# Kernel optimization log

Hardware: AMD Instinct MI355X
Metric: run time of the kernel (lower is better)

The kernel has to match this reference:

```python
import jax, jax.numpy as jnp
import numpy as np

B, S, D = 1, 2048, 1024          # batch, seq, n_embd
E, F = 16, 1024                  # n_routed_experts, moe_intermediate_size
NG, TKG, K = 4, 2, 4             # n_group, topk_group, num_experts_per_tok
NSH = 2                          # n_shared_experts
SCALE = 2.5                      # routed_scaling_factor
STD = 0.02
EPG = E // NG                    # experts per group


def setup_inputs() -> dict:
    key = jax.random.key(0)
    ks = jax.random.split(key, 8)
    return {
        "hidden_states": jax.random.normal(ks[0], (B, S, D), jnp.float32),
        "router_w": jax.random.normal(ks[1], (E, D), jnp.float32) * STD,   # gate.weight
        "bias": jnp.zeros((E,), jnp.float32),                              # e_score_correction_bias
        "gate_w": jax.random.normal(ks[2], (E, D, F), jnp.float32) * STD,  # per-expert gate_proj (transposed)
        "up_w": jax.random.normal(ks[3], (E, D, F), jnp.float32) * STD,    # per-expert up_proj
        "down_w": jax.random.normal(ks[4], (E, F, D), jnp.float32) * STD,  # per-expert down_proj
        "sh_gate_w": jax.random.normal(ks[5], (D, NSH * F), jnp.float32) * STD,
        "sh_up_w": jax.random.normal(ks[6], (D, NSH * F), jnp.float32) * STD,
        "sh_down_w": jax.random.normal(ks[7], (NSH * F, D), jnp.float32) * STD,
    }


def _route(x_flat, router_w, bias):
    # x_flat: [T, D] -> topk_idx [T, K], topk_w [T, K]
    logits = x_flat.astype(jnp.float32) @ router_w.T          # [T, E]
    scores = jax.nn.sigmoid(logits)
    s = scores + bias[None, :]                                # scores_for_choice
    sg = s.reshape(-1, NG, EPG)
    group_score = jax.lax.top_k(sg, 2)[0].sum(-1)             # sum of top-2 per group [T, NG]
    gidx = jax.lax.top_k(group_score, TKG)[1]                 # [T, TKG]
    gmask = jnp.sum(jax.nn.one_hot(gidx, NG, dtype=jnp.float32), axis=1) > 0   # [T, NG]
    emask = jnp.repeat(gmask, EPG, axis=1)                    # [T, E]
    masked = jnp.where(emask, s, -1.0)
    topk_idx = jax.lax.top_k(masked, K)[1]                    # [T, K]
    tw = jnp.take_along_axis(scores, topk_idx, axis=1)        # gather raw sigmoid scores
    tw = tw / (tw.sum(-1, keepdims=True) + 1e-20)             # norm_topk_prob
    tw = tw * SCALE
    return topk_idx, tw


def reference(hidden_states, router_w, bias, gate_w, up_w, down_w,
              sh_gate_w, sh_up_w, sh_down_w):
    x = hidden_states.reshape(-1, D)                          # [T, D]
    topk_idx, tw = _route(x, router_w, bias)
    # combine weights per (token, expert): scatter-add of topk weights
    combine = (jax.nn.one_hot(topk_idx, E, dtype=tw.dtype) * tw[..., None]).sum(1)  # [T, E]
    # per-expert SwiGLU MLPs (dense dispatch, masked combine == index_add semantics)
    h = jnp.einsum('td,edf->etf', x, gate_w)                  # [E, T, F]
    u = jnp.einsum('td,edf->etf', x, up_w)
    y = jnp.einsum('etf,efd->etd', jax.nn.silu(h) * u, down_w)  # [E, T, D]
    routed = jnp.einsum('etd,te->td', y, combine)             # weighted combine
    # shared experts
    sh = (jax.nn.silu(x @ sh_gate_w) * (x @ sh_up_w)) @ sh_down_w
    return (routed + sh).reshape(hidden_states.shape)
```

## Files before the change

### kernel.cpp

```cpp
#include <hip/hip_runtime.h>
#include <cstdint>
#include <cstddef>


#define T_TOK 2048
#define DIM   1024
#define NEXP  16
#define MAXTILES 80
#define SH_TILES 32
#define GRID_Y (MAXTILES + SH_TILES)
#define ABASE_SH 10240

typedef __bf16 bf16x8_t __attribute__((ext_vector_type(8)));
typedef float  f32x4_t  __attribute__((ext_vector_type(4)));
typedef unsigned short ushort8_t __attribute__((ext_vector_type(8)));
typedef unsigned short ushort4_t __attribute__((ext_vector_type(4)));

#define OFF_XB     (0UL)
#define OFF_SHGT   (4UL<<20)
#define OFF_SHUT   (8UL<<20)
#define OFF_GATET  (12UL<<20)
#define OFF_UPT    (44UL<<20)
#define OFF_DOWNT  (76UL<<20)
#define OFF_SHDT   (108UL<<20)
#define OFF_ACT    (112UL<<20)
#define OFF_YSLOT  (140UL<<20)
#define OFF_PART   (0UL)
#define OFF_CTRL   (160UL<<20)
#define CT_OFFSETS  128
#define CT_NTILES   192
#define CT_TILEEXP  256
#define CT_SLOTTOK  4096
#define CT_TKSLOT   49152
#define CT_TOPKIDX  81920
#define CT_TOPKW    114688

__device__ __forceinline__ unsigned short f2bf(float f) {
  __bf16 h = (__bf16)f;
  return __builtin_bit_cast(unsigned short, h);
}
__device__ __forceinline__ float bf2f(unsigned short u) {
  unsigned int v = ((unsigned int)u) << 16;
  return __builtin_bit_cast(float, v);
}
__device__ __forceinline__ void gld16(const void* g, void* l) {
  __builtin_amdgcn_global_load_lds(
      (const __attribute__((address_space(1))) void*)(g),
      (__attribute__((address_space(3))) void*)(l), 16, 0, 0);
}

__global__ void k_cvt(const float* __restrict__ src, unsigned short* __restrict__ dst, int n4) {
  int i = blockIdx.x * blockDim.x + threadIdx.x;
  if (i >= n4) return;
  float4 v = ((const float4*)src)[i];
  ushort4_t o;
  o[0] = f2bf(v.x); o[1] = f2bf(v.y); o[2] = f2bf(v.z); o[3] = f2bf(v.w);
  ((ushort4_t*)dst)[i] = o;
}

__global__ void k_transpose(const float* __restrict__ src, unsigned short* __restrict__ dst,
                            int R, int C) {
  __shared__ unsigned short tile[64 * 68];
  long b = blockIdx.z;
  src += b * (long)R * C;
  dst += b * (long)R * C;
  int cT = blockIdx.x * 64, rT = blockIdx.y * 64;
  int t = threadIdx.x;
  int rb = t >> 4, cb = t & 15;
  float f[4][4];
#pragma unroll
  for (int i = 0; i < 4; i++) {
    float4 v = *(const float4*)(src + (long)(rT + 4 * rb + i) * C + cT + 4 * cb);
    f[i][0] = v.x; f[i][1] = v.y; f[i][2] = v.z; f[i][3] = v.w;
  }
#pragma unroll
  for (int j = 0; j < 4; j++) {
    ushort4_t o;
    o[0] = f2bf(f[0][j]); o[1] = f2bf(f[1][j]); o[2] = f2bf(f[2][j]); o[3] = f2bf(f[3][j]);
    int c = 4 * cb + j;
    *(ushort4_t*)&tile[c * 68 + 4 * rb] = o;
  }
  __syncthreads();
#pragma unroll
  for (int p = 0; p < 2; p++) {
    int q = t + 256 * p;
    int c = q >> 3, r0 = (q & 7) * 8;
    ushort4_t lo = *(const ushort4_t*)&tile[c * 68 + r0];
    ushort4_t hi = *(const ushort4_t*)&tile[c * 68 + r0 + 4];
    ushort8_t w8 = {lo[0], lo[1], lo[2], lo[3], hi[0], hi[1], hi[2], hi[3]};
    *(ushort8_t*)(dst + (long)(cT + c) * R + rT + r0) = w8;
  }
}

__global__ __launch_bounds__(256) void k_router(
    const float* __restrict__ x, const float* __restrict__ rw,
    const float* __restrict__ bias, int* __restrict__ topk_idx,
    float* __restrict__ topk_w) {
  int t = blockIdx.x, tid = threadIdx.x;
  int wv = tid >> 6, lane = tid & 63;
  float4 xv = ((const float4*)(x + (size_t)t * DIM))[tid];
  float part[NEXP];
#pragma unroll
  for (int e = 0; e < NEXP; e++) {
    float4 wr = ((const float4*)(rw + (size_t)e * DIM))[tid];
    part[e] = xv.x * wr.x + xv.y * wr.y + xv.z * wr.z + xv.w * wr.w;
  }
  __shared__ float wsum_s[4 * NEXP];
#pragma unroll
  for (int e = 0; e < NEXP; e++) {
    float v = part[e];
#pragma unroll
    for (int off = 32; off; off >>= 1) v += __shfl_xor(v, off, 64);
    if (lane == 0) wsum_s[wv * NEXP + e] = v;
  }
  __syncthreads();
  if (tid == 0) {
    float r_sc[NEXP], r_s[NEXP];
#pragma unroll
    for (int e = 0; e < NEXP; e++) {
      float logit = wsum_s[e] + wsum_s[NEXP + e] + wsum_s[2 * NEXP + e] +
                    wsum_s[3 * NEXP + e];
      float sc = 1.f / (1.f + expf(-logit));
      r_sc[e] = sc;
      r_s[e] = sc + bias[e];
    }
    float gs[4];
#pragma unroll
    for (int g = 0; g < 4; g++) {
      float m1 = -1e30f, m2 = -1e30f;
#pragma unroll
      for (int j = 0; j < 4; j++) {
        float v = r_s[g * 4 + j];
        if (v > m1) { m2 = m1; m1 = v; } else if (v > m2) m2 = v;
      }
      gs[g] = m1 + m2;
    }
    int g1 = 0;
    for (int g = 1; g < 4; g++) if (gs[g] > gs[g1]) g1 = g;
    int g2 = -1;
    for (int g = 0; g < 4; g++) { if (g == g1) continue; if (g2 < 0 || gs[g] > gs[g2]) g2 = g; }
    int taken = 0, idx[4];
    float w[4], wsum = 1e-20f;
#pragma unroll
    for (int k = 0; k < 4; k++) {
      float best = -1e30f; int bi = 0;
#pragma unroll
      for (int e2 = 0; e2 < 16; e2++) {
        if (taken & (1 << e2)) continue;
        int g = e2 >> 2;
        float v = (g == g1 || g == g2) ? r_s[e2] : -1.f;
        if (v > best) { best = v; bi = e2; }
      }
      taken |= 1 << bi; idx[k] = bi;
    }
#pragma unroll
    for (int k = 0; k < 4; k++) { w[k] = r_sc[idx[k]]; wsum += w[k]; }
    float sc2 = 2.5f / wsum;
#pragma unroll
    for (int k = 0; k < 4; k++) {
      topk_idx[t * 4 + k] = idx[k];
      topk_w[t * 4 + k] = w[k] * sc2;
    }
  }
}

__global__ __launch_bounds__(256) void k_route_post(
    const int* __restrict__ topk_idx, int* __restrict__ offsets,
    int* __restrict__ tile_expert, int* __restrict__ n_tiles,
    int* __restrict__ slot_token, int* __restrict__ tk_slot) {
  __shared__ int cnt[NEXP][257];
  __shared__ int offs[NEXP], tot[NEXP];
  int tid = threadIdx.x;
  int4 ent[8];
#pragma unroll
  for (int i = 0; i < 8; i++) ent[i] = ((const int4*)topk_idx)[tid * 8 + i];
  int lc[NEXP];
#pragma unroll
  for (int j = 0; j < NEXP; j++) lc[j] = 0;
#pragma unroll
  for (int i = 0; i < 8; i++) {
    int es[4] = {ent[i].x, ent[i].y, ent[i].z, ent[i].w};
#pragma unroll
    for (int k = 0; k < 4; k++)
#pragma unroll
      for (int j = 0; j < NEXP; j++) lc[j] += (es[k] == j) ? 1 : 0;
  }
#pragma unroll
  for (int j = 0; j < NEXP; j++) cnt[j][tid] = lc[j];
  __syncthreads();
  if (tid < NEXP) {
    int base = 0;
    for (int c = 0; c < 256; c += 8) {
      int v[8];
#pragma unroll
      for (int i = 0; i < 8; i++) v[i] = cnt[tid][c + i];
#pragma unroll
      for (int i = 0; i < 8; i++) { cnt[tid][c + i] = base; base += v[i]; }
    }
    tot[tid] = base;
  }
  __syncthreads();
  if (tid == 0) {
    int cum = 0, tt = 0;
    for (int e = 0; e < NEXP; e++) {
      offs[e] = cum;
      offsets[e] = cum;
      int nt = (tot[e] + 127) >> 7;
      for (int i = 0; i < nt; i++) tile_expert[tt++] = e;
      cum += nt << 7;
    }
    n_tiles[0] = tt;
  }
  __syncthreads();
  for (int e = 0; e < NEXP; e++) {
    int s0 = offs[e] + tot[e];
    int s1 = offs[e] + (((tot[e] + 127) >> 7) << 7);
    for (int s = s0 + tid; s < s1; s += 256) slot_token[s] = -1;
  }
  int lcur[NEXP];
#pragma unroll
  for (int j = 0; j < NEXP; j++) lcur[j] = offs[j] + cnt[j][tid];
#pragma unroll
  for (int i = 0; i < 8; i++) {
    int t = tid * 8 + i;
    int es[4] = {ent[i].x, ent[i].y, ent[i].z, ent[i].w};
#pragma unroll
    for (int k = 0; k < 4; k++) {
      int e = es[k], pos = 0;
#pragma unroll
      for (int j = 0; j < NEXP; j++) pos += (e == j) ? lcur[j] : 0;
#pragma unroll
      for (int j = 0; j < NEXP; j++) lcur[j] += (e == j) ? 1 : 0;
      slot_token[pos] = t;
      tk_slot[t * 4 + k] = pos;
    }
  }
}

__global__ __launch_bounds__(256, 2) void k_gateup(
    const unsigned short* __restrict__ xb, const unsigned short* __restrict__ gateT,
    const unsigned short* __restrict__ upT, const unsigned short* __restrict__ shGT,
    const unsigned short* __restrict__ shUT, unsigned short* __restrict__ act,
    const int* __restrict__ slot_token, const int* __restrict__ tile_expert,
    const int* __restrict__ n_tiles) {
  int nx = blockIdx.x, bt = blockIdx.y;
  int NT = n_tiles[0];
  bool routed = bt < NT;
  const unsigned short *Bg, *Bu;
  int actbase, tokbase = 0;
  if (routed) {
    int e = tile_expert[bt];
    Bg = gateT + ((size_t)e << 20);
    Bu = upT + ((size_t)e << 20);
    actbase = bt * 128;
  } else {
    int st = bt - NT;
    if (st >= SH_TILES) return;
    int se = st >> 4, tt = st & 15;
    Bg = shGT + ((size_t)se << 20);
    Bu = shUT + ((size_t)se << 20);
    actbase = ABASE_SH + se * T_TOK + tt * 128;
    tokbase = tt * 128;
  }
  int n0 = nx * 128;

  __shared__ unsigned short sA[128 * 32];
  __shared__ unsigned short sBg[128 * 32];
  __shared__ unsigned short sBu[128 * 32];

  int tid = threadIdx.x;
  int w = tid >> 6, L = tid & 63;
  int c0 = w * 128 + L, c1 = c0 + 64;
  int ar0 = c0 >> 2, ar1 = c1 >> 2;
  int ch0 = (c0 & 3) ^ (ar0 & 3), ch1 = (c1 & 3) ^ (ar1 & 3);
  long arow0, arow1;
  if (routed) {
    int t0 = slot_token[bt * 128 + ar0]; if (t0 < 0) t0 = 0;
    int t1 = slot_token[bt * 128 + ar1]; if (t1 < 0) t1 = 0;
    arow0 = t0; arow1 = t1;
  } else {
    arow0 = tokbase + ar0; arow1 = tokbase + ar1;
  }
  const char* aA = (const char*)(xb + arow0 * 1024) + ch0 * 16;
  const char* aB = (const char*)(xb + arow1 * 1024) + ch1 * 16;
  const char* gA = (const char*)(Bg + (size_t)(n0 + ar0) * 1024) + ch0 * 16;
  const char* gB = (const char*)(Bg + (size_t)(n0 + ar1) * 1024) + ch1 * 16;
  const char* uA = (const char*)(Bu + (size_t)(n0 + ar0) * 1024) + ch0 * 16;
  const char* uB = (const char*)(Bu + (size_t)(n0 + ar1) * 1024) + ch1 * 16;
  char* dA0 = (char*)sA + (w * 128) * 16;
  char* dA1 = (char*)sA + (w * 128 + 64) * 16;
  char* dG0 = (char*)sBg + (w * 128) * 16;
  char* dG1 = (char*)sBg + (w * 128 + 64) * 16;
  char* dU0 = (char*)sBu + (w * 128) * 16;
  char* dU1 = (char*)sBu + (w * 128 + 64) * 16;

  f32x4_t accg[4][4], accu[4][4];
#pragma unroll
  for (int i = 0; i < 4; i++)
#pragma unroll
    for (int j = 0; j < 4; j++) {
      accg[i][j] = f32x4_t{0.f, 0.f, 0.f, 0.f};
      accu[i][j] = f32x4_t{0.f, 0.f, 0.f, 0.f};
    }

  int mb = (w >> 1) * 64, nb = (w & 1) * 64;
  int lr = L & 15, quad = L >> 4;
  int sw = ((quad ^ (lr & 3)) << 3);

  for (int kt = 0; kt < 32; ++kt) {
    gld16(aA, dA0); gld16(aB, dA1);
    gld16(gA, dG0); gld16(gB, dG1);
    gld16(uA, dU0); gld16(uB, dU1);
    aA += 64; aB += 64; gA += 64; gB += 64; uA += 64; uB += 64;
    __syncthreads();
    bf16x8_t af[4], bg[4], bu[4];
#pragma unroll
    for (int i = 0; i < 4; i++) af[i] = *(const bf16x8_t*)(sA + (mb + 16 * i + lr) * 32 + sw);
#pragma unroll
    for (int i = 0; i < 4; i++) bg[i] = *(const bf16x8_t*)(sBg + (nb + 16 * i + lr) * 32 + sw);
#pragma unroll
    for (int i = 0; i < 4; i++) bu[i] = *(const bf16x8_t*)(sBu + (nb + 16 * i + lr) * 32 + sw);
#pragma unroll
    for (int i = 0; i < 4; i++)
#pragma unroll
      for (int j = 0; j < 4; j++) {
        accg[i][j] = __builtin_amdgcn_mfma_f32_16x16x32_bf16(af[i], bg[j], accg[i][j], 0, 0, 0);
        accu[i][j] = __builtin_amdgcn_mfma_f32_16x16x32_bf16(af[i], bu[j], accu[i][j], 0, 0, 0);
      }
    __syncthreads();
  }

#pragma unroll
  for (int i = 0; i < 4; i++) {
    int rowb = actbase + mb + 16 * i + quad * 4;
#pragma unroll
    for (int j = 0; j < 4; j++) {
      int col = n0 + nb + 16 * j + lr;
#pragma unroll
      for (int r = 0; r < 4; r++) {
        float h = accg[i][j][r];
        float u = accu[i][j][r];
        float a = h / (1.f + __expf(-h)) * u;
        act[(size_t)(rowb + r) * 1024 + col] = f2bf(a);
      }
    }
  }
}

__global__ __launch_bounds__(256, 2) void k_down(
    const unsigned short* __restrict__ act, const unsigned short* __restrict__ downT,
    const unsigned short* __restrict__ shDT, unsigned short* __restrict__ yslot,
    float* __restrict__ part, const int* __restrict__ tile_expert,
    const int* __restrict__ n_tiles) {
  int nx = blockIdx.x, bt = blockIdx.y;
  int NT = n_tiles[0];
  bool routed = bt < NT;
  const unsigned short* B;
  size_t bstride;
  int abase, obase, se = 0;
  if (routed) {
    int e = tile_expert[bt];
    B = downT + ((size_t)e << 20);
    bstride = 1024;
    abase = bt * 128;
    obase = bt * 128;
  } else {
    int st = bt - NT;
    if (st >= SH_TILES) return;
    se = st >> 4;
    int tt = st & 15;
    B = shDT + se * 1024;
    bstride = 2048;
    abase = ABASE_SH + se * T_TOK + tt * 128;
    obase = tt * 128;
  }
  int n0 = nx * 128;

  __shared__ unsigned short sA[128 * 32];
  __shared__ unsigned short sB[128 * 32];

  int tid = threadIdx.x;
  int w = tid >> 6, L = tid & 63;
  int c0 = w * 128 + L, c1 = c0 + 64;
  int ar0 = c0 >> 2, ar1 = c1 >> 2;
  int ch0 = (c0 & 3) ^ (ar0 & 3), ch1 = (c1 & 3) ^ (ar1 & 3);
  const char* aA = (const char*)(act + (size_t)(abase + ar0) * 1024) + ch0 * 16;
  const char* aB = (const char*)(act + (size_t)(abase + ar1) * 1024) + ch1 * 16;
  const char* bA = (const char*)(B + (size_t)(n0 + ar0) * bstride) + ch0 * 16;
  const char* bB = (const char*)(B + (size_t)(n0 + ar1) * bstride) + ch1 * 16;
  char* dA0 = (char*)sA + (w * 128) * 16;
  char* dA1 = (char*)sA + (w * 128 + 64) * 16;
  char* dB0 = (char*)sB + (w * 128) * 16;
  char* dB1 = (char*)sB + (w * 128 + 64) * 16;

  f32x4_t acc[4][4];
#pragma unroll
  for (int i = 0; i < 4; i++)
#pragma unroll
    for (int j = 0; j < 4; j++) acc[i][j] = f32x4_t{0.f, 0.f, 0.f, 0.f};

  int mb = (w >> 1) * 64, nb = (w & 1) * 64;
  int lr = L & 15, quad = L >> 4;
  int sw = ((quad ^ (lr & 3)) << 3);

  for (int kt = 0; kt < 32; ++kt) {
    gld16(aA, dA0); gld16(aB, dA1);
    gld16(bA, dB0); gld16(bB, dB1);
    aA += 64; aB += 64; bA += 64; bB += 64;
    __syncthreads();
    bf16x8_t af[4], bf[4];
#pragma unroll
    for (int i = 0; i < 4; i++) af[i] = *(const bf16x8_t*)(sA + (mb + 16 * i + lr) * 32 + sw);
#pragma unroll
    for (int i = 0; i < 4; i++) bf[i] = *(const bf16x8_t*)(sB + (nb + 16 * i + lr) * 32 + sw);
#pragma unroll
    for (int i = 0; i < 4; i++)
#pragma unroll
      for (int j = 0; j < 4; j++)
        acc[i][j] = __builtin_amdgcn_mfma_f32_16x16x32_bf16(af[i], bf[j], acc[i][j], 0, 0, 0);
    __syncthreads();
  }

#pragma unroll
  for (int i = 0; i < 4; i++) {
    int rowb = obase + mb + 16 * i + quad * 4;
#pragma unroll
    for (int j = 0; j < 4; j++) {
      int col = n0 + nb + 16 * j + lr;
#pragma unroll
      for (int r = 0; r < 4; r++) {
        float v = acc[i][j][r];
        if (routed) yslot[(size_t)(rowb + r) * 1024 + col] = f2bf(v);
        else part[(size_t)se * (T_TOK * 1024) + (size_t)(rowb + r) * 1024 + col] = v;
      }
    }
  }
}

__global__ void k_gather(float* __restrict__ out, const float* __restrict__ partial,
                         const unsigned short* __restrict__ yslot,
                         const int* __restrict__ tk_slot, const float* __restrict__ topk_w) {
  int t = blockIdx.x, tid = threadIdx.x;
  int4 sl = ((const int4*)tk_slot)[t];
  float4 wv = ((const float4*)topk_w)[t];
  int d = 4 * tid;
  float4 p0 = *(const float4*)(partial + (size_t)t * 1024 + d);
  float4 p1 = *(const float4*)(partial + (size_t)(T_TOK * 1024) + (size_t)t * 1024 + d);
  float4 o = {p0.x + p1.x, p0.y + p1.y, p0.z + p1.z, p0.w + p1.w};
  const int s[4] = {sl.x, sl.y, sl.z, sl.w};
  const float wk[4] = {wv.x, wv.y, wv.z, wv.w};
#pragma unroll
  for (int k = 0; k < 4; k++) {
    ushort4_t y = *(const ushort4_t*)(yslot + (size_t)s[k] * 1024 + d);
    o.x += wk[k] * bf2f(y[0]);
    o.y += wk[k] * bf2f(y[1]);
    o.z += wk[k] * bf2f(y[2]);
    o.w += wk[k] * bf2f(y[3]);
  }
  *(float4*)(out + (size_t)t * 1024 + d) = o;
}

extern "C" void kernel_launch(void* const* d_in, const int* in_sizes, int n_in,
                              void* d_out, int out_size, void* d_ws, size_t ws_size,
                              hipStream_t stream) {
  const float* x = (const float*)d_in[0];
  const float* rw = (const float*)d_in[1];
  const float* bias = (const float*)d_in[2];
  const float* gw = (const float*)d_in[3];
  const float* uw = (const float*)d_in[4];
  const float* dw = (const float*)d_in[5];
  const float* sg = (const float*)d_in[6];
  const float* su = (const float*)d_in[7];
  const float* sd = (const float*)d_in[8];
  float* out = (float*)d_out;
  char* ws = (char*)d_ws;

  unsigned short* xb    = (unsigned short*)(ws + OFF_XB);
  unsigned short* shGT  = (unsigned short*)(ws + OFF_SHGT);
  unsigned short* shUT  = (unsigned short*)(ws + OFF_SHUT);
  unsigned short* gateT = (unsigned short*)(ws + OFF_GATET);
  unsigned short* upT   = (unsigned short*)(ws + OFF_UPT);
  unsigned short* downT = (unsigned short*)(ws + OFF_DOWNT);
  unsigned short* shDT  = (unsigned short*)(ws + OFF_SHDT);
  unsigned short* act   = (unsigned short*)(ws + OFF_ACT);
  unsigned short* yslot = (unsigned short*)(ws + OFF_YSLOT);
  float*          part  = (float*)(ws + OFF_PART);
  char* ctrl = ws + OFF_CTRL;
  int* offsets_    = (int*)(ctrl + CT_OFFSETS);
  int* n_tiles     = (int*)(ctrl + CT_NTILES);
  int* tile_expert = (int*)(ctrl + CT_TILEEXP);
  int* slot_token  = (int*)(ctrl + CT_SLOTTOK);
  int* tk_slot     = (int*)(ctrl + CT_TKSLOT);
  int* topk_idx    = (int*)(ctrl + CT_TOPKIDX);
  float* topk_w    = (float*)(ctrl + CT_TOPKW);

  k_cvt<<<2048, 256, 0, stream>>>(x, xb, T_TOK * DIM / 4);
  k_transpose<<<dim3(16, 16, 16), 256, 0, stream>>>(gw, gateT, 1024, 1024);
  k_transpose<<<dim3(16, 16, 16), 256, 0, stream>>>(uw, upT, 1024, 1024);
  k_transpose<<<dim3(16, 16, 16), 256, 0, stream>>>(dw, downT, 1024, 1024);
  k_transpose<<<dim3(32, 16, 1), 256, 0, stream>>>(sg, shGT, 1024, 2048);
  k_transpose<<<dim3(32, 16, 1), 256, 0, stream>>>(su, shUT, 1024, 2048);
  k_transpose<<<dim3(16, 32, 1), 256, 0, stream>>>(sd, shDT, 2048, 1024);
  k_router<<<2048, 256, 0, stream>>>(x, rw, bias, topk_idx, topk_w);
  k_route_post<<<1, 256, 0, stream>>>(topk_idx, offsets_, tile_expert, n_tiles,
                                      slot_token, tk_slot);
  k_gateup<<<dim3(8, GRID_Y), 256, 0, stream>>>(xb, gateT, upT, shGT, shUT, act,
                                                slot_token, tile_expert, n_tiles);
  k_down<<<dim3(8, GRID_Y), 256, 0, stream>>>(act, downT, shDT, yslot, part,
                                              tile_expert, n_tiles);
  k_gather<<<2048, 256, 0, stream>>>(out, part, yslot, tk_slot, topk_w);
}
```

Before: 433.6 us.

## Double-buffer LDS in MoE GEMMs, remap block order, fuse weight transpose launches

```diff
diff --git a/kernel.cpp b/kernel.cpp
--- a/kernel.cpp
+++ b/kernel.cpp
@@ -9,6 +9,7 @@
 #define MAXTILES 80
 #define SH_TILES 32
 #define GRID_Y (MAXTILES + SH_TILES)
+#define NBLK (8 * GRID_Y)
 #define ABASE_SH 10240
 
 typedef __bf16 bf16x8_t __attribute__((ext_vector_type(8)));
@@ -49,21 +50,10 @@
       (__attribute__((address_space(3))) void*)(l), 16, 0, 0);
 }
 
-__global__ void k_cvt(const float* __restrict__ src, unsigned short* __restrict__ dst, int n4) {
-  int i = blockIdx.x * blockDim.x + threadIdx.x;
-  if (i >= n4) return;
-  float4 v = ((const float4*)src)[i];
-  ushort4_t o;
-  o[0] = f2bf(v.x); o[1] = f2bf(v.y); o[2] = f2bf(v.z); o[3] = f2bf(v.w);
-  ((ushort4_t*)dst)[i] = o;
-}
-
-__global__ void k_transpose(const float* __restrict__ src, unsigned short* __restrict__ dst,
-                            int R, int C) {
+__device__ __forceinline__ void tbody(const float* __restrict__ src,
+                                      unsigned short* __restrict__ dst,
+                                      int R, int C) {
   __shared__ unsigned short tile[64 * 68];
-  long b = blockIdx.z;
-  src += b * (long)R * C;
-  dst += b * (long)R * C;
   int cT = blockIdx.x * 64, rT = blockIdx.y * 64;
   int t = threadIdx.x;
   int rb = t >> 4, cb = t & 15;
@@ -92,13 +82,40 @@
   }
 }
 
+__global__ void k_transpose(const float* __restrict__ src, unsigned short* __restrict__ dst,
+                            int R, int C) {
+  long b = blockIdx.z;
+  tbody(src + b * (long)R * C, dst + b * (long)R * C, R, C);
+}
+
+__global__ void k_transpose3(const float* __restrict__ g, const float* __restrict__ u,
+                             const float* __restrict__ d, unsigned short* __restrict__ gT,
+                             unsigned short* __restrict__ uT, unsigned short* __restrict__ dT) {
+  int z = blockIdx.z;
+  int which = z >> 4;
+  long b = z & 15;
+  const float* s = (which == 0) ? g : (which == 1) ? u : d;
+  unsigned short* t = (which == 0) ? gT : (which == 1) ? uT : dT;
+  tbody(s + b * 1048576L, t + b * 1048576L, 1024, 1024);
+}
+
+__global__ void k_transpose_sh(const float* __restrict__ sg, const float* __restrict__ su,
+                               unsigned short* __restrict__ gT, unsigned short* __restrict__ uT) {
+  const float* s = blockIdx.z ? su : sg;
+  unsigned short* t = blockIdx.z ? uT : gT;
+  tbody(s, t, 1024, 2048);
+}
+
 __global__ __launch_bounds__(256) void k_router(
     const float* __restrict__ x, const float* __restrict__ rw,
     const float* __restrict__ bias, int* __restrict__ topk_idx,
-    float* __restrict__ topk_w) {
+    float* __restrict__ topk_w, unsigned short* __restrict__ xb) {
   int t = blockIdx.x, tid = threadIdx.x;
   int wv = tid >> 6, lane = tid & 63;
   float4 xv = ((const float4*)(x + (size_t)t * DIM))[tid];
+  ushort4_t xo;
+  xo[0] = f2bf(xv.x); xo[1] = f2bf(xv.y); xo[2] = f2bf(xv.z); xo[3] = f2bf(xv.w);
+  ((ushort4_t*)(xb + (size_t)t * DIM))[tid] = xo;
   float part[NEXP];
 #pragma unroll
   for (int e = 0; e < NEXP; e++) {
@@ -243,7 +260,9 @@
     const unsigned short* __restrict__ shUT, unsigned short* __restrict__ act,
     const int* __restrict__ slot_token, const int* __restrict__ tile_expert,
     const int* __restrict__ n_tiles) {
-  int nx = blockIdx.x, bt = blockIdx.y;
+  int o = blockIdx.x;
+  int wk = (o & 7) * GRID_Y + (o >> 3);
+  int nx = wk & 7, bt = wk >> 3;
   int NT = n_tiles[0];
   bool routed = bt < NT;
   const unsigned short *Bg, *Bu;
@@ -264,9 +283,7 @@
   }
   int n0 = nx * 128;
 
-  __shared__ unsigned short sA[128 * 32];
-  __shared__ unsigned short sBg[128 * 32];
-  __shared__ unsigned short sBu[128 * 32];
+  __shared__ unsigned short lds[2 * 3 * 128 * 32];
 
   int tid = threadIdx.x;
   int w = tid >> 6, L = tid & 63;
@@ -287,12 +304,9 @@
   const char* gB = (const char*)(Bg + (size_t)(n0 + ar1) * 1024) + ch1 * 16;
   const char* uA = (const char*)(Bu + (size_t)(n0 + ar0) * 1024) + ch0 * 16;
   const char* uB = (const char*)(Bu + (size_t)(n0 + ar1) * 1024) + ch1 * 16;
-  char* dA0 = (char*)sA + (w * 128) * 16;
-  char* dA1 = (char*)sA + (w * 128 + 64) * 16;
-  char* dG0 = (char*)sBg + (w * 128) * 16;
-  char* dG1 = (char*)sBg + (w * 128 + 64) * 16;
-  char* dU0 = (char*)sBu + (w * 128) * 16;
-  char* dU1 = (char*)sBu + (w * 128 + 64) * 16;
+  const int a0o = w * 2048, a1o = w * 2048 + 1024;
+  const int g0o = 8192 + w * 2048, g1o = 8192 + w * 2048 + 1024;
+  const int u0o = 16384 + w * 2048, u1o = 16384 + w * 2048 + 1024;
 
   f32x4_t accg[4][4], accu[4][4];
 #pragma unroll
@@ -307,28 +321,43 @@
   int lr = L & 15, quad = L >> 4;
   int sw = ((quad ^ (lr & 3)) << 3);
 
-  for (int kt = 0; kt < 32; ++kt) {
-    gld16(aA, dA0); gld16(aB, dA1);
-    gld16(gA, dG0); gld16(gB, dG1);
-    gld16(uA, dU0); gld16(uB, dU1);
-    aA += 64; aB += 64; gA += 64; gB += 64; uA += 64; uB += 64;
-    __syncthreads();
-    bf16x8_t af[4], bg[4], bu[4];
-#pragma unroll
-    for (int i = 0; i < 4; i++) af[i] = *(const bf16x8_t*)(sA + (mb + 16 * i + lr) * 32 + sw);
-#pragma unroll
-    for (int i = 0; i < 4; i++) bg[i] = *(const bf16x8_t*)(sBg + (nb + 16 * i + lr) * 32 + sw);
-#pragma unroll
-    for (int i = 0; i < 4; i++) bu[i] = *(const bf16x8_t*)(sBu + (nb + 16 * i + lr) * 32 + sw);
-#pragma unroll
-    for (int i = 0; i < 4; i++)
-#pragma unroll
-      for (int j = 0; j < 4; j++) {
-        accg[i][j] = __builtin_amdgcn_mfma_f32_16x16x32_bf16(af[i], bg[j], accg[i][j], 0, 0, 0);
-        accu[i][j] = __builtin_amdgcn_mfma_f32_16x16x32_bf16(af[i], bu[j], accu[i][j], 0, 0, 0);
-      }
-    __syncthreads();
-  }
+#define GU_STAGE(BOFF)                                                       \
+  { char* bp = (char*)lds + (BOFF);                                          \
+    gld16(aA, bp + a0o); gld16(aB, bp + a1o);                                \
+    gld16(gA, bp + g0o); gld16(gB, bp + g1o);                                \
+    gld16(uA, bp + u0o); gld16(uB, bp + u1o);                                \
+    aA += 64; aB += 64; gA += 64; gB += 64; uA += 64; uB += 64; }
+
+#define GU_COMPUTE(UOFF)                                                     \
+  { const unsigned short* pA = lds + (UOFF);                                 \
+    const unsigned short* pG = pA + 4096;                                    \
+    const unsigned short* pU = pA + 8192;                                    \
+    bf16x8_t af[4], bg[4], bu[4];                                            \
+    _Pragma("unroll")                                                        \
+    for (int i = 0; i < 4; i++) af[i] = *(const bf16x8_t*)(pA + (mb + 16 * i + lr) * 32 + sw); \
+    _Pragma("unroll")                                                        \
+    for (int i = 0; i < 4; i++) bg[i] = *(const bf16x8_t*)(pG + (nb + 16 * i + lr) * 32 + sw); \
+    _Pragma("unroll")                                                        \
+    for (int i = 0; i < 4; i++) bu[i] = *(const bf16x8_t*)(pU + (nb + 16 * i + lr) * 32 + sw); \
+    _Pragma("unroll")                                                        \
+    for (int i = 0; i < 4; i++)                                              \
+      _Pragma("unroll")                                                      \
+      for (int j = 0; j < 4; j++) {                                          \
+        accg[i][j] = __builtin_amdgcn_mfma_f32_16x16x32_bf16(af[i], bg[j], accg[i][j], 0, 0, 0); \
+        accu[i][j] = __builtin_amdgcn_mfma_f32_16x16x32_bf16(af[i], bu[j], accu[i][j], 0, 0, 0); \
+      } }
+
+  GU_STAGE(0);
+  __syncthreads();
+#pragma unroll 1
+  for (int p = 0; p < 15; ++p) {
+    GU_STAGE(24576); GU_COMPUTE(0);     __syncthreads();
+    GU_STAGE(0);     GU_COMPUTE(12288); __syncthreads();
+  }
+  GU_STAGE(24576); GU_COMPUTE(0); __syncthreads();
+  GU_COMPUTE(12288);
+#undef GU_STAGE
+#undef GU_COMPUTE
 
 #pragma unroll
   for (int i = 0; i < 4; i++) {
@@ -352,7 +381,9 @@
     const unsigned short* __restrict__ shDT, unsigned short* __restrict__ yslot,
     float* __restrict__ part, const int* __restrict__ tile_expert,
     const int* __restrict__ n_tiles) {
-  int nx = blockIdx.x, bt = blockIdx.y;
+  int o = blockIdx.x;
+  int wk = (o & 7) * GRID_Y + (o >> 3);
+  int nx = wk & 7, bt = wk >> 3;
   int NT = n_tiles[0];
   bool routed = bt < NT;
   const unsigned short* B;
@@ -376,8 +407,7 @@
   }
   int n0 = nx * 128;
 
-  __shared__ unsigned short sA[128 * 32];
-  __shared__ unsigned short sB[128 * 32];
+  __shared__ unsigned short lds[2 * 2 * 128 * 32];
 
   int tid = threadIdx.x;
   int w = tid >> 6, L = tid & 63;
@@ -388,10 +418,8 @@
   const char* aB = (const char*)(act + (size_t)(abase + ar1) * 1024) + ch1 * 16;
   const char* bA = (const char*)(B + (size_t)(n0 + ar0) * bstride) + ch0 * 16;
   const char* bB = (const char*)(B + (size_t)(n0 + ar1) * bstride) + ch1 * 16;
-  char* dA0 = (char*)sA + (w * 128) * 16;
-  char* dA1 = (char*)sA + (w * 128 + 64) * 16;
-  char* dB0 = (char*)sB + (w * 128) * 16;
-  char* dB1 = (char*)sB + (w * 128 + 64) * 16;
+  const int a0o = w * 2048, a1o = w * 2048 + 1024;
+  const int b0o = 8192 + w * 2048, b1o = 8192 + w * 2048 + 1024;
 
   f32x4_t acc[4][4];
 #pragma unroll
@@ -403,23 +431,37 @@
   int lr = L & 15, quad = L >> 4;
   int sw = ((quad ^ (lr & 3)) << 3);
 
-  for (int kt = 0; kt < 32; ++kt) {
-    gld16(aA, dA0); gld16(aB, dA1);
-    gld16(bA, dB0); gld16(bB, dB1);
-    aA += 64; aB += 64; bA += 64; bB += 64;
-    __syncthreads();
-    bf16x8_t af[4], bf[4];
-#pragma unroll
-    for (int i = 0; i < 4; i++) af[i] = *(const bf16x8_t*)(sA + (mb + 16 * i + lr) * 32 + sw);
-#pragma unroll
-    for (int i = 0; i < 4; i++) bf[i] = *(const bf16x8_t*)(sB + (nb + 16 * i + lr) * 32 + sw);
-#pragma unroll
-    for (int i = 0; i < 4; i++)
-#pragma unroll
-      for (int j = 0; j < 4; j++)
-        acc[i][j] = __builtin_amdgcn_mfma_f32_16x16x32_bf16(af[i], bf[j], acc[i][j], 0, 0, 0);
-    __syncthreads();
-  }
+#define DN_STAGE(BOFF)                                                       \
+  { char* bp = (char*)lds + (BOFF);                                          \
+    gld16(aA, bp + a0o); gld16(aB, bp + a1o);                                \
+    gld16(bA, bp + b0o); gld16(bB, bp + b1o);                                \
+    aA += 64; aB += 64; bA += 64; bB += 64; }
+
+#define DN_COMPUTE(UOFF)                                                     \
+  { const unsigned short* pA = lds + (UOFF);                                 \
+    const unsigned short* pB = pA + 4096;                                    \
+    bf16x8_t af[4], bb[4];                                                   \
+    _Pragma("unroll")                                                        \
+    for (int i = 0; i < 4; i++) af[i] = *(const bf16x8_t*)(pA + (mb + 16 * i + lr) * 32 + sw); \
+    _Pragma("unroll")                                                        \
+    for (int i = 0; i < 4; i++) bb[i] = *(const bf16x8_t*)(pB + (nb + 16 * i + lr) * 32 + sw); \
+    _Pragma("unroll")                                                        \
+    for (int i = 0; i < 4; i++)                                              \
+      _Pragma("unroll")                                                      \
+      for (int j = 0; j < 4; j++)                                            \
+        acc[i][j] = __builtin_amdgcn_mfma_f32_16x16x32_bf16(af[i], bb[j], acc[i][j], 0, 0, 0); }
+
+  DN_STAGE(0);
+  __syncthreads();
+#pragma unroll 1
+  for (int p = 0; p < 15; ++p) {
+    DN_STAGE(16384); DN_COMPUTE(0);    __syncthreads();
+    DN_STAGE(0);     DN_COMPUTE(8192); __syncthreads();
+  }
+  DN_STAGE(16384); DN_COMPUTE(0); __syncthreads();
+  DN_COMPUTE(8192);
+#undef DN_STAGE
+#undef DN_COMPUTE
 
 #pragma unroll
   for (int i = 0; i < 4; i++) {
@@ -494,19 +536,15 @@
   int* topk_idx    = (int*)(ctrl + CT_TOPKIDX);
   float* topk_w    = (float*)(ctrl + CT_TOPKW);
 
-  k_cvt<<<2048, 256, 0, stream>>>(x, xb, T_TOK * DIM / 4);
-  k_transpose<<<dim3(16, 16, 16), 256, 0, stream>>>(gw, gateT, 1024, 1024);
-  k_transpose<<<dim3(16, 16, 16), 256, 0, stream>>>(uw, upT, 1024, 1024);
-  k_transpose<<<dim3(16, 16, 16), 256, 0, stream>>>(dw, downT, 1024, 1024);
-  k_transpose<<<dim3(32, 16, 1), 256, 0, stream>>>(sg, shGT, 1024, 2048);
-  k_transpose<<<dim3(32, 16, 1), 256, 0, stream>>>(su, shUT, 1024, 2048);
+  k_transpose3<<<dim3(16, 16, 48), 256, 0, stream>>>(gw, uw, dw, gateT, upT, downT);
+  k_transpose_sh<<<dim3(32, 16, 2), 256, 0, stream>>>(sg, su, shGT, shUT);
   k_transpose<<<dim3(16, 32, 1), 256, 0, stream>>>(sd, shDT, 2048, 1024);
-  k_router<<<2048, 256, 0, stream>>>(x, rw, bias, topk_idx, topk_w);
+  k_router<<<2048, 256, 0, stream>>>(x, rw, bias, topk_idx, topk_w, xb);
   k_route_post<<<1, 256, 0, stream>>>(topk_idx, offsets_, tile_expert, n_tiles,
                                       slot_token, tk_slot);
-  k_gateup<<<dim3(8, GRID_Y), 256, 0, stream>>>(xb, gateT, upT, shGT, shUT, act,
-                                                slot_token, tile_expert, n_tiles);
-  k_down<<<dim3(8, GRID_Y), 256, 0, stream>>>(act, downT, shDT, yslot, part,
-                                              tile_expert, n_tiles);
+  k_gateup<<<NBLK, 256, 0, stream>>>(xb, gateT, upT, shGT, shUT, act,
+                                     slot_token, tile_expert, n_tiles);
+  k_down<<<NBLK, 256, 0, stream>>>(act, downT, shDT, yslot, part,
+                                   tile_expert, n_tiles);
   k_gather<<<2048, 256, 0, stream>>>(out, part, yslot, tk_slot, topk_w);
 }
```

Result: faster. 418.0 us (-3.6%).
